# Kernel tuning notes

Hardware: AMD Instinct MI355X
Metric: run time of the kernel (lower is better)

Reference implementation:

```python
import jax, jax.numpy as jnp
import numpy as np

B = 524288   # number of samples scored at inference
K = 8        # GMM mixture components
D = 16       # latent feature dim (AE code + reconstruction-error features)


def setup_inputs() -> dict:
    key = jax.random.key(0)
    k1, k2, k3, k4 = jax.random.split(key, 4)
    z = jax.random.normal(k1, (B, D), dtype=jnp.float32)
    mu = jax.random.normal(k2, (K, D), dtype=jnp.float32)
    # sigma must be SPD (it is an estimated covariance + 0.001*I in the original);
    # build it as A A^T / D + 0.1*I so cholesky succeeds and densities are sane.
    A = jax.random.normal(k3, (K, D, D), dtype=jnp.float32) / np.sqrt(D)
    sigma = jnp.einsum('kij,klj->kil', A, A) + 0.1 * jnp.eye(D, dtype=jnp.float32)
    logits = jax.random.normal(k4, (K,), dtype=jnp.float32)
    mixture_probabilities = jax.nn.softmax(logits)
    return {"mu": mu, "sigma": sigma, "z": z,
            "mixture_probabilities": mixture_probabilities}


def reference(mu, sigma, z, mixture_probabilities):
    # Faithful to compute_sample_energy: per-sample MVN density for each of K
    # components via Cholesky, weighted by mixture probs, summed, -log.
    # Vectorized: one batched triangular solve instead of tf.map_fn per sample.
    d = z.shape[-1]
    L = jnp.linalg.cholesky(sigma)                      # [K,D,D]
    diff = z[:, None, :] - mu[None, :, :]               # [B,K,D]
    diff_t = jnp.transpose(diff, (1, 2, 0))             # [K,D,B]
    y = jax.scipy.linalg.solve_triangular(L, diff_t, lower=True)  # [K,D,B]
    maha = jnp.sum(y * y, axis=1)                       # [K,B] Mahalanobis dist
    log_det = jnp.sum(jnp.log(jnp.diagonal(L, axis1=-2, axis2=-1)), axis=-1)  # [K]
    log_norm = -0.5 * d * jnp.log(jnp.asarray(2.0 * np.pi, dtype=z.dtype))
    log_prob = log_norm - log_det[:, None] - 0.5 * maha  # [K,B]
    densities = jnp.exp(log_prob).T                      # [B,K] == map_fn(prob)
    energy = -jnp.log(jnp.sum(densities * mixture_probabilities, axis=1))  # [B]
    return energy
```

## Files before the change

### kernel.cpp

```cpp
#include <hip/hip_runtime.h>
#include <math.h>

#define KCOMP 8
#define DDIM  16

typedef __attribute__((ext_vector_type(8))) short bf16x8;
typedef __attribute__((ext_vector_type(4))) float f32x4;

static __device__ __forceinline__ short f2bf(float f) {
    unsigned u = __float_as_uint(f);
    unsigned r = (u + 0x7FFFu + ((u >> 16) & 1u)) >> 16;
    return (short)r;
}

__global__ __launch_bounds__(256) void dagmm_kernel(
    const float* __restrict__ mu, const float* __restrict__ sigma,
    const float* __restrict__ pi, const float* __restrict__ z,
    float* __restrict__ out, int n)
{
    __shared__ float sLinv[KCOMP * DDIM * DDIM];
    __shared__ float sB[KCOMP * DDIM];
    __shared__ float sC[KCOMP];

    const int tid = threadIdx.x;

    if (tid < 128) {
        const int g = tid >> 4;
        const int r = tid & 15;

        float a[DDIM];
        const float4* srow = (const float4*)(sigma + g * DDIM * DDIM + r * DDIM);
        float4 v0 = srow[0], v1 = srow[1], v2 = srow[2], v3 = srow[3];
        a[0]=v0.x;  a[1]=v0.y;  a[2]=v0.z;  a[3]=v0.w;
        a[4]=v1.x;  a[5]=v1.y;  a[6]=v1.z;  a[7]=v1.w;
        a[8]=v2.x;  a[9]=v2.y;  a[10]=v2.z; a[11]=v2.w;
        a[12]=v3.x; a[13]=v3.y; a[14]=v3.z; a[15]=v3.w;

        float l[DDIM];
        #pragma unroll
        for (int j = 0; j < DDIM; ++j) {
            float s = a[j];
            #pragma unroll
            for (int m2 = 0; m2 < j; ++m2)
                s -= l[m2] * __shfl(l[m2], j, DDIM);
            float dj = sqrtf(__shfl(s, j, DDIM));
            float val;
            if (r == j)      val = dj;
            else if (r > j)  val = s / dj;
            else             val = 0.0f;
            l[j] = val;
        }

        float x[DDIM];
        #pragma unroll
        for (int i = 0; i < DDIM; ++i) {
            float t = (r == i) ? 1.0f : 0.0f;
            #pragma unroll
            for (int m2 = 0; m2 < i; ++m2)
                t -= __shfl(l[m2], i, DDIM) * x[m2];
            x[i] = t / __shfl(l[i], i, DDIM);
        }

        #pragma unroll
        for (int i = 0; i < DDIM; ++i)
            sLinv[g * 256 + i * DDIM + r] = x[i];

        float b = 0.0f;
        #pragma unroll
        for (int c = 0; c < DDIM; ++c)
            b += sLinv[g * 256 + r * DDIM + c] * mu[g * DDIM + c];
        sB[g * DDIM + r] = b;

        float ld = logf(l[r]);
        #pragma unroll
        for (int off = 8; off >= 1; off >>= 1)
            ld += __shfl_xor(ld, off, DDIM);
        if (r == 0) {
            const float LOG2PI = 1.8378770664093454f;
            sC[g] = logf(pi[g]) - ld - 0.5f * DDIM * LOG2PI;
        }
    }
    __syncthreads();

    const int lane = tid & 63;
    const int m    = lane & 15;
    const int quad = lane >> 4;
    const int wave = (blockIdx.x * 256 + tid) >> 6;

    bf16x8 afrag[KCOMP];
    #pragma unroll
    for (int k = 0; k < KCOMP; ++k) {
        bf16x8 a = {0,0,0,0,0,0,0,0};
        if (quad < 2) {
            const float* Lrow = &sLinv[k * 256 + m * DDIM + quad * 8];
            #pragma unroll
            for (int j = 0; j < 8; ++j) a[j] = f2bf(Lrow[j]);
        } else if (quad == 2) {
            a[0] = f2bf(-sB[k * DDIM + m]);
        }
        afrag[k] = a;
    }
    float ck[KCOMP];
    #pragma unroll
    for (int k = 0; k < KCOMP; ++k) ck[k] = sC[k];

    const f32x4 zero4 = {0.f, 0.f, 0.f, 0.f};
    const int base = wave * 256;

    #pragma unroll 1
    for (int it = 0; it < 4; ++it) {
        const int tb = base + it * 64;
        float pk[4][KCOMP];

        #pragma unroll
        for (int t = 0; t < 4; ++t) {
            bf16x8 bfrag = {0,0,0,0,0,0,0,0};
            const int s = tb + t * 16 + m;
            if (quad < 2) {
                if (s < n) {
                    const float* zp = z + (size_t)s * DDIM + quad * 8;
                    #pragma unroll
                    for (int j = 0; j < 8; ++j) bfrag[j] = f2bf(zp[j]);
                }
            } else if (quad == 2) {
                bfrag[0] = (short)0x3F80;
            }

            #pragma unroll
            for (int k = 0; k < KCOMP; ++k) {
                f32x4 d4 = __builtin_amdgcn_mfma_f32_16x16x32_bf16(
                               afrag[k], bfrag, zero4, 0, 0, 0);
                float p = d4[0]*d4[0] + d4[1]*d4[1] + d4[2]*d4[2] + d4[3]*d4[3];
                p += __shfl_xor(p, 16, 64);
                p += __shfl_xor(p, 32, 64);
                pk[t][k] = p;
            }
        }

        float lp[KCOMP];
        #pragma unroll
        for (int k = 0; k < KCOMP; ++k) {
            float p = pk[0][k];
            p = (quad == 1) ? pk[1][k] : p;
            p = (quad == 2) ? pk[2][k] : p;
            p = (quad == 3) ? pk[3][k] : p;
            lp[k] = fmaf(-0.5f, p, ck[k]);
        }
        float mx = lp[0];
        #pragma unroll
        for (int k = 1; k < KCOMP; ++k) mx = fmaxf(mx, lp[k]);
        float dens = 0.0f;
        #pragma unroll
        for (int k = 0; k < KCOMP; ++k) dens += __expf(lp[k] - mx);

        const int so = tb + quad * 16 + m;
        if (so < n) out[so] = -(mx + __logf(dens));
    }
}

extern "C" void kernel_launch(void* const* d_in, const int* in_sizes, int n_in,
                              void* d_out, int out_size, void* d_ws, size_t ws_size,
                              hipStream_t stream) {
    const float* mu    = (const float*)d_in[0];
    const float* sigma = (const float*)d_in[1];
    const float* z     = (const float*)d_in[2];
    const float* pi    = (const float*)d_in[3];
    float* out = (float*)d_out;
    (void)d_ws; (void)ws_size;

    const int n = in_sizes[2] / DDIM;

    const int blocks = (n + 1023) / 1024;
    dagmm_kernel<<<blocks, 256, 0, stream>>>(mu, sigma, pi, z, out, n);
}
```

Before: 113.4 us.

## Split Cholesky prep into a single-block kernel and slim the MFMA energy kernel

The Cholesky factorisation, triangular inverse and bf16 fragment packing move into a one-block prep kernel that writes packed A-fragments and per-component constants to workspace. Before, every energy block repeated that serial per-block setup. The energy kernel now loads the fragments directly, processes 64 samples per wave instead of 256 so it launches four times as many blocks, and loads z with float4 reads. The cost is an extra kernel launch and a serial dependency on the tiny prep kernel.

```diff
diff --git a/kernel.cpp b/kernel.cpp
--- a/kernel.cpp
+++ b/kernel.cpp
@@ -7,155 +7,170 @@
 typedef __attribute__((ext_vector_type(8))) short bf16x8;
 typedef __attribute__((ext_vector_type(4))) float f32x4;
 
-static __device__ __forceinline__ short f2bf(float f) {
+static __device__ __forceinline__ unsigned short f2bf(float f) {
     unsigned u = __float_as_uint(f);
     unsigned r = (u + 0x7FFFu + ((u >> 16) & 1u)) >> 16;
-    return (short)r;
+    return (unsigned short)r;
 }
 
-__global__ __launch_bounds__(256) void dagmm_kernel(
+__global__ __launch_bounds__(128) void prep_kernel(
     const float* __restrict__ mu, const float* __restrict__ sigma,
-    const float* __restrict__ pi, const float* __restrict__ z,
-    float* __restrict__ out, int n)
+    const float* __restrict__ pi, float* __restrict__ ws)
 {
     __shared__ float sLinv[KCOMP * DDIM * DDIM];
     __shared__ float sB[KCOMP * DDIM];
     __shared__ float sC[KCOMP];
 
     const int tid = threadIdx.x;
+    const int g = tid >> 4;
+    const int r = tid & 15;
 
-    if (tid < 128) {
-        const int g = tid >> 4;
-        const int r = tid & 15;
+    float a[DDIM];
+    const float4* srow = (const float4*)(sigma + g * DDIM * DDIM + r * DDIM);
+    float4 v0 = srow[0], v1 = srow[1], v2 = srow[2], v3 = srow[3];
+    a[0]=v0.x;  a[1]=v0.y;  a[2]=v0.z;  a[3]=v0.w;
+    a[4]=v1.x;  a[5]=v1.y;  a[6]=v1.z;  a[7]=v1.w;
+    a[8]=v2.x;  a[9]=v2.y;  a[10]=v2.z; a[11]=v2.w;
+    a[12]=v3.x; a[13]=v3.y; a[14]=v3.z; a[15]=v3.w;
 
-        float a[DDIM];
-        const float4* srow = (const float4*)(sigma + g * DDIM * DDIM + r * DDIM);
-        float4 v0 = srow[0], v1 = srow[1], v2 = srow[2], v3 = srow[3];
-        a[0]=v0.x;  a[1]=v0.y;  a[2]=v0.z;  a[3]=v0.w;
-        a[4]=v1.x;  a[5]=v1.y;  a[6]=v1.z;  a[7]=v1.w;
-        a[8]=v2.x;  a[9]=v2.y;  a[10]=v2.z; a[11]=v2.w;
-        a[12]=v3.x; a[13]=v3.y; a[14]=v3.z; a[15]=v3.w;
+    float l[DDIM];
+    #pragma unroll
+    for (int j = 0; j < DDIM; ++j) {
+        float s = a[j];
+        #pragma unroll
+        for (int m2 = 0; m2 < j; ++m2)
+            s -= l[m2] * __shfl(l[m2], j, DDIM);
+        float dj = sqrtf(__shfl(s, j, DDIM));
+        float val;
+        if (r == j)      val = dj;
+        else if (r > j)  val = s / dj;
+        else             val = 0.0f;
+        l[j] = val;
+    }
 
-        float l[DDIM];
+    float x[DDIM];
+    #pragma unroll
+    for (int i = 0; i < DDIM; ++i) {
+        float t = (r == i) ? 1.0f : 0.0f;
         #pragma unroll
-        for (int j = 0; j < DDIM; ++j) {
-            float s = a[j];
-            #pragma unroll
-            for (int m2 = 0; m2 < j; ++m2)
-                s -= l[m2] * __shfl(l[m2], j, DDIM);
-            float dj = sqrtf(__shfl(s, j, DDIM));
-            float val;
-            if (r == j)      val = dj;
-            else if (r > j)  val = s / dj;
-            else             val = 0.0f;
-            l[j] = val;
-        }
+        for (int m2 = 0; m2 < i; ++m2)
+            t -= __shfl(l[m2], i, DDIM) * x[m2];
+        x[i] = t / __shfl(l[i], i, DDIM);
+    }
 
-        float x[DDIM];
-        #pragma unroll
-        for (int i = 0; i < DDIM; ++i) {
-            float t = (r == i) ? 1.0f : 0.0f;
-            #pragma unroll
-            for (int m2 = 0; m2 < i; ++m2)
-                t -= __shfl(l[m2], i, DDIM) * x[m2];
-            x[i] = t / __shfl(l[i], i, DDIM);
-        }
+    #pragma unroll
+    for (int i = 0; i < DDIM; ++i)
+        sLinv[g * 256 + i * DDIM + r] = x[i];
 
-        #pragma unroll
-        for (int i = 0; i < DDIM; ++i)
-            sLinv[g * 256 + i * DDIM + r] = x[i];
+    float b = 0.0f;
+    #pragma unroll
+    for (int c = 0; c < DDIM; ++c)
+        b += sLinv[g * 256 + r * DDIM + c] * mu[g * DDIM + c];
+    sB[g * DDIM + r] = b;
 
-        float b = 0.0f;
-        #pragma unroll
-        for (int c = 0; c < DDIM; ++c)
-            b += sLinv[g * 256 + r * DDIM + c] * mu[g * DDIM + c];
-        sB[g * DDIM + r] = b;
-
-        float ld = logf(l[r]);
-        #pragma unroll
-        for (int off = 8; off >= 1; off >>= 1)
-            ld += __shfl_xor(ld, off, DDIM);
-        if (r == 0) {
-            const float LOG2PI = 1.8378770664093454f;
-            sC[g] = logf(pi[g]) - ld - 0.5f * DDIM * LOG2PI;
-        }
+    float ld = logf(l[r]);
+    #pragma unroll
+    for (int off = 8; off >= 1; off >>= 1)
+        ld += __shfl_xor(ld, off, DDIM);
+    if (r == 0) {
+        const float LOG2PI = 1.8378770664093454f;
+        sC[g] = logf(pi[g]) - ld - 0.5f * DDIM * LOG2PI;
     }
     __syncthreads();
 
+    #pragma unroll
+    for (int i = 0; i < 4; ++i) {
+        const int e    = tid + i * 128;
+        const int k    = e >> 6;
+        const int lane = e & 63;
+        const int m    = lane & 15;
+        const int quad = lane >> 4;
+        float vals[8];
+        #pragma unroll
+        for (int j = 0; j < 8; ++j) vals[j] = 0.0f;
+        if (quad < 2) {
+            #pragma unroll
+            for (int j = 0; j < 8; ++j)
+                vals[j] = sLinv[k * 256 + m * DDIM + quad * 8 + j];
+        } else if (quad == 2) {
+            vals[0] = -sB[k * DDIM + m];
+        }
+        uint4 p;
+        p.x = (unsigned)f2bf(vals[0]) | ((unsigned)f2bf(vals[1]) << 16);
+        p.y = (unsigned)f2bf(vals[2]) | ((unsigned)f2bf(vals[3]) << 16);
+        p.z = (unsigned)f2bf(vals[4]) | ((unsigned)f2bf(vals[5]) << 16);
+        p.w = (unsigned)f2bf(vals[6]) | ((unsigned)f2bf(vals[7]) << 16);
+        ((uint4*)ws)[e] = p;
+    }
+    if (tid < KCOMP) ws[2048 + tid] = sC[tid];
+}
+
+__global__ __launch_bounds__(256, 4) void energy_kernel(
+    const float* __restrict__ z, const float* __restrict__ ws,
+    float* __restrict__ out, int n)
+{
+    const int tid  = threadIdx.x;
     const int lane = tid & 63;
     const int m    = lane & 15;
     const int quad = lane >> 4;
-    const int wave = (blockIdx.x * 256 + tid) >> 6;
+    const int base = ((blockIdx.x * 256 + tid) >> 6) * 64;
 
     bf16x8 afrag[KCOMP];
     #pragma unroll
-    for (int k = 0; k < KCOMP; ++k) {
-        bf16x8 a = {0,0,0,0,0,0,0,0};
-        if (quad < 2) {
-            const float* Lrow = &sLinv[k * 256 + m * DDIM + quad * 8];
-            #pragma unroll
-            for (int j = 0; j < 8; ++j) a[j] = f2bf(Lrow[j]);
-        } else if (quad == 2) {
-            a[0] = f2bf(-sB[k * DDIM + m]);
-        }
-        afrag[k] = a;
-    }
+    for (int k = 0; k < KCOMP; ++k)
+        afrag[k] = ((const bf16x8*)ws)[k * 64 + lane];
+
     float ck[KCOMP];
     #pragma unroll
-    for (int k = 0; k < KCOMP; ++k) ck[k] = sC[k];
+    for (int k = 0; k < KCOMP; ++k) ck[k] = ws[2048 + k];
+
+    bf16x8 bfrag[4];
+    #pragma unroll
+    for (int t = 0; t < 4; ++t) {
+        bf16x8 bf = {0,0,0,0,0,0,0,0};
+        const int s = base + t * 16 + m;
+        if (quad < 2) {
+            if (s < n) {
+                const float4* zp = (const float4*)(z + (size_t)s * DDIM + quad * 8);
+                float4 w0 = zp[0], w1 = zp[1];
+                bf[0]=(short)f2bf(w0.x); bf[1]=(short)f2bf(w0.y);
+                bf[2]=(short)f2bf(w0.z); bf[3]=(short)f2bf(w0.w);
+                bf[4]=(short)f2bf(w1.x); bf[5]=(short)f2bf(w1.y);
+                bf[6]=(short)f2bf(w1.z); bf[7]=(short)f2bf(w1.w);
+            }
+        } else if (quad == 2) {
+            bf[0] = (short)0x3F80;
+        }
+        bfrag[t] = bf;
+    }
 
     const f32x4 zero4 = {0.f, 0.f, 0.f, 0.f};
-    const int base = wave * 256;
+    float lp[KCOMP];
 
-    #pragma unroll 1
-    for (int it = 0; it < 4; ++it) {
-        const int tb = base + it * 64;
-        float pk[4][KCOMP];
-
-        #pragma unroll
-        for (int t = 0; t < 4; ++t) {
-            bf16x8 bfrag = {0,0,0,0,0,0,0,0};
-            const int s = tb + t * 16 + m;
-            if (quad < 2) {
-                if (s < n) {
-                    const float* zp = z + (size_t)s * DDIM + quad * 8;
-                    #pragma unroll
-                    for (int j = 0; j < 8; ++j) bfrag[j] = f2bf(zp[j]);
-                }
-            } else if (quad == 2) {
-                bfrag[0] = (short)0x3F80;
-            }
-
-            #pragma unroll
-            for (int k = 0; k < KCOMP; ++k) {
-                f32x4 d4 = __builtin_amdgcn_mfma_f32_16x16x32_bf16(
-                               afrag[k], bfrag, zero4, 0, 0, 0);
-                float p = d4[0]*d4[0] + d4[1]*d4[1] + d4[2]*d4[2] + d4[3]*d4[3];
-                p += __shfl_xor(p, 16, 64);
-                p += __shfl_xor(p, 32, 64);
-                pk[t][k] = p;
-            }
-        }
-
-        float lp[KCOMP];
+    #pragma unroll
+    for (int t = 0; t < 4; ++t) {
         #pragma unroll
         for (int k = 0; k < KCOMP; ++k) {
-            float p = pk[0][k];
-            p = (quad == 1) ? pk[1][k] : p;
-            p = (quad == 2) ? pk[2][k] : p;
-            p = (quad == 3) ? pk[3][k] : p;
-            lp[k] = fmaf(-0.5f, p, ck[k]);
+            f32x4 d4 = __builtin_amdgcn_mfma_f32_16x16x32_bf16(
+                           afrag[k], bfrag[t], zero4, 0, 0, 0);
+            float p = d4[0]*d4[0] + d4[1]*d4[1] + d4[2]*d4[2] + d4[3]*d4[3];
+            p += __shfl_xor(p, 16, 64);
+            p += __shfl_xor(p, 32, 64);
+            float lpv = fmaf(-0.5f, p, ck[k]);
+            if (t == 0) lp[k] = lpv;
+            else        lp[k] = (quad == t) ? lpv : lp[k];
         }
-        float mx = lp[0];
-        #pragma unroll
-        for (int k = 1; k < KCOMP; ++k) mx = fmaxf(mx, lp[k]);
-        float dens = 0.0f;
-        #pragma unroll
-        for (int k = 0; k < KCOMP; ++k) dens += __expf(lp[k] - mx);
+    }
 
-        const int so = tb + quad * 16 + m;
-        if (so < n) out[so] = -(mx + __logf(dens));
-    }
+    float mx = lp[0];
+    #pragma unroll
+    for (int k = 1; k < KCOMP; ++k) mx = fmaxf(mx, lp[k]);
+    float dens = 0.0f;
+    #pragma unroll
+    for (int k = 0; k < KCOMP; ++k) dens += __expf(lp[k] - mx);
+
+    const int so = base + lane;
+    if (so < n) out[so] = -(mx + __logf(dens));
 }
 
 extern "C" void kernel_launch(void* const* d_in, const int* in_sizes, int n_in,
@@ -165,11 +180,13 @@
     const float* sigma = (const float*)d_in[1];
     const float* z     = (const float*)d_in[2];
     const float* pi    = (const float*)d_in[3];
+    float* ws  = (float*)d_ws;
     float* out = (float*)d_out;
-    (void)d_ws; (void)ws_size;
 
     const int n = in_sizes[2] / DDIM;
 
-    const int blocks = (n + 1023) / 1024;
-    dagmm_kernel<<<blocks, 256, 0, stream>>>(mu, sigma, pi, z, out, n);
+    prep_kernel<<<1, 128, 0, stream>>>(mu, sigma, pi, ws);
+
+    const int blocks = (n + 255) / 256;
+    energy_kernel<<<blocks, 256, 0, stream>>>(z, ws, out, n);
 }
```

New measurement: 94.44 us. 16.7% less time.
